# Performance work log

Hardware: AMD Instinct MI355X
Metric: run time of the kernel (lower is better)

Reference implementation:

```python
import jax, jax.numpy as jnp
import numpy as np

NEG_SLOPE = 0.2  # PyG GATv2Conv default
HEADS = 3


def setup_inputs() -> dict:
    key = jax.random.key(0)
    ks = jax.random.split(key, 5)
    N, D, H, C = 16384, 128, HEADS, 128
    x = jax.random.normal(ks[0], (N, D), dtype=jnp.float32)
    Wl = jax.random.normal(ks[1], (D, H * C), dtype=jnp.float32) * (1.0 / np.sqrt(D))
    Wr = jax.random.normal(ks[2], (D, H * C), dtype=jnp.float32) * (1.0 / np.sqrt(D))
    att = jax.random.normal(ks[3], (H, C), dtype=jnp.float32) * (1.0 / np.sqrt(C))
    bias = jnp.zeros((C,), dtype=jnp.float32)
    return {"x": x, "Wl": Wl, "Wr": Wr, "att": att, "bias": bias, "k": 16}


def _knn_indices(x, k):
    # squared euclidean pairwise distances, exclude self (loop=False)
    sq = jnp.sum(x * x, axis=1)
    dist = sq[:, None] + sq[None, :] - 2.0 * (x @ x.T)  # [N, N]
    n = x.shape[0]
    ar = jnp.arange(n)
    dist = dist.at[ar, ar].set(jnp.inf)
    _, idx = jax.lax.top_k(-dist, k)  # [N, k] neighbor (source) indices per target node
    return idx


def reference(x, Wl, Wr, att, bias, k):
    N = x.shape[0]
    H = att.shape[0]
    C = att.shape[1]
    idx = _knn_indices(x, k)                     # [N, k]
    xl = (x @ Wl).reshape(N, H, C)               # source transform
    xr = (x @ Wr).reshape(N, H, C)               # target transform
    xl_nbr = xl[idx]                             # [N, k, H, C] gathered source feats
    g = jax.nn.leaky_relu(xl_nbr + xr[:, None], NEG_SLOPE)
    e = jnp.einsum('nkhc,hc->nkh', g, att)       # per-edge attention logits
    alpha = jax.nn.softmax(e, axis=1)            # softmax over the k neighbors of each target
    out = jnp.einsum('nkh,nkhc->nhc', alpha, xl_nbr)
    return out.mean(axis=1) + bias               # concat=False: mean over heads, then bias
```

## Files before the change

### kernel.cpp

```cpp
#include <hip/hip_runtime.h>
#include <math.h>

#define N_NODES 16384
#define DIM 128
#define HC 384
#define NEG_SLOPE 0.2f
#define KNN 16
#define KP2 6
#define NSEG 8
#define NCAND 192
#define SEGC (N_NODES / NSEG)
#define TILES32 (SEGC / 32)
#define LROW 272
#define LBUF2 (32 * LROW)

typedef _Float16 f16x8 __attribute__((ext_vector_type(8)));
typedef _Float16 f16x2 __attribute__((ext_vector_type(2)));
typedef float f32x4 __attribute__((ext_vector_type(4)));
typedef unsigned long long u64;

__global__ __launch_bounds__(256) void prep_x(const float* __restrict__ x,
                                              float* __restrict__ sq,
                                              _Float16* __restrict__ xhi,
                                              _Float16* __restrict__ xlo) {
  const int wv = threadIdx.x >> 6;
  const int lane = threadIdx.x & 63;
  const int row = blockIdx.x * 4 + wv;
  const float2 v = *(const float2*)&x[row * DIM + lane * 2];
  float s = v.x * v.x + v.y * v.y;
  #pragma unroll
  for (int off = 32; off > 0; off >>= 1) s += __shfl_down(s, off);
  _Float16 h0 = (_Float16)v.x, h1 = (_Float16)v.y;
  _Float16 l0 = (_Float16)(v.x - (float)h0), l1 = (_Float16)(v.y - (float)h1);
  f16x2 hh; hh[0] = h0; hh[1] = h1;
  f16x2 ll; ll[0] = l0; ll[1] = l1;
  *(f16x2*)&xhi[row * DIM + lane * 2] = hh;
  *(f16x2*)&xlo[row * DIM + lane * 2] = ll;
  if (lane == 0) sq[row] = s;
}

__global__ __launch_bounds__(256) void prep_w(const float* __restrict__ Wl,
                                              const float* __restrict__ Wr,
                                              _Float16* __restrict__ wthi,
                                              _Float16* __restrict__ wtlo) {
  const int t = blockIdx.x * 256 + threadIdx.x;
  const int mat = t / 49152;
  const int e = t - mat * 49152;
  const int k = e / HC;
  const int c = e - k * HC;
  const float w = (mat ? Wr : Wl)[e];
  _Float16 h = (_Float16)w;
  _Float16 l = (_Float16)(w - (float)h);
  wthi[mat * 49152 + c * DIM + k] = h;
  wtlo[mat * 49152 + c * DIM + k] = l;
}

__global__ __launch_bounds__(256) void gemm_xw_mfma(const _Float16* __restrict__ xhi,
                                                    const _Float16* __restrict__ xlo,
                                                    const _Float16* __restrict__ wthi,
                                                    const _Float16* __restrict__ wtlo,
                                                    _Float16* __restrict__ xl,
                                                    _Float16* __restrict__ xr) {
  const int lane = threadIdx.x & 63;
  const int wid = blockIdx.x * 4 + (threadIdx.x >> 6);
  const int mat = wid / 6144;
  const int rem = wid - mat * 6144;
  const int rt = rem / 6;
  const int ctg = rem - rt * 6;
  const int r0 = lane & 15;
  const int g8 = (lane >> 4) * 8;

  const _Float16* ap_hi = xhi + (size_t)(rt * 16 + r0) * DIM + g8;
  const _Float16* ap_lo = xlo + (size_t)(rt * 16 + r0) * DIM + g8;
  f16x8 ah[4], al[4];
  #pragma unroll
  for (int ks = 0; ks < 4; ks++) {
    ah[ks] = *(const f16x8*)(ap_hi + ks * 32);
    al[ks] = *(const f16x8*)(ap_lo + ks * 32);
  }
  _Float16* o = mat ? xr : xl;

  #pragma unroll
  for (int ct4 = 0; ct4 < 4; ct4++) {
    const int ct = ctg * 4 + ct4;
    const _Float16* bp_hi = wthi + mat * 49152 + (ct * 16 + r0) * DIM + g8;
    const _Float16* bp_lo = wtlo + mat * 49152 + (ct * 16 + r0) * DIM + g8;
    f32x4 acc = {0.f, 0.f, 0.f, 0.f};
    #pragma unroll
    for (int ks = 0; ks < 4; ks++) {
      f16x8 bh = *(const f16x8*)(bp_hi + ks * 32);
      f16x8 bl = *(const f16x8*)(bp_lo + ks * 32);
      acc = __builtin_amdgcn_mfma_f32_16x16x32_f16(ah[ks], bh, acc, 0, 0, 0);
      acc = __builtin_amdgcn_mfma_f32_16x16x32_f16(ah[ks], bl, acc, 0, 0, 0);
      acc = __builtin_amdgcn_mfma_f32_16x16x32_f16(al[ks], bh, acc, 0, 0, 0);
    }
    #pragma unroll
    for (int i = 0; i < 4; i++) {
      const int row = rt * 16 + (lane >> 4) * 4 + i;
      o[(size_t)row * HC + ct * 16 + r0] = (_Float16)acc[i];
    }
  }
}

__device__ __forceinline__ unsigned umin32(unsigned a, unsigned b) { return a < b ? a : b; }
__device__ __forceinline__ unsigned umax32(unsigned a, unsigned b) { return a > b ? a : b; }

__device__ __forceinline__ void ripple(unsigned pk, unsigned* pool) {
  unsigned cur = pk;
  #pragma unroll
  for (int s = 0; s < KP2; s++) {
    const unsigned mn = umin32(cur, pool[s]);
    cur = umax32(cur, pool[s]);
    pool[s] = mn;
  }
}

__device__ __forceinline__ void insert4s(const f32x4 acc, const f32x4 scv,
                                         int cb_cg, int selfid, unsigned* pool) {
  unsigned k0, k1, k2, k3;
  {
    unsigned kk[4];
    #pragma unroll
    for (int r = 0; r < 4; r++) {
      const int cid = cb_cg + r;
      const float key = fmaf(-2.f, acc[r], scv[r]);
      unsigned u = __float_as_uint(key);
      u ^= (unsigned)(((int)u >> 31) | 0x80000000u);
      unsigned pk = (u & 0xFFFFC000u) | (unsigned)cid;
      kk[r] = (cid == selfid) ? 0xFFFFFFFFu : pk;
    }
    k0 = kk[0]; k1 = kk[1]; k2 = kk[2]; k3 = kk[3];
  }
  #define CSWAP(a, b) { const unsigned mn = umin32(a, b), mx = umax32(a, b); a = mn; b = mx; }
  CSWAP(k0, k1) CSWAP(k2, k3) CSWAP(k0, k2) CSWAP(k1, k3) CSWAP(k1, k2)
  #undef CSWAP
  ripple(k0, pool);
  if (k1 < pool[KP2 - 1]) {
    ripple(k1, pool);
    ripple(k2, pool);
    ripple(k3, pool);
  }
}

__global__ __launch_bounds__(256, 8) void knn_kernel(const _Float16* __restrict__ xhi,
                                                     const float* __restrict__ sq,
                                                     int* __restrict__ cand) {
  __shared__ __align__(16) char lds[2 * LBUF2];

  const int lane = threadIdx.x & 63;
  const int w = threadIdx.x >> 6;
  const int seg = __builtin_amdgcn_readfirstlane(blockIdx.x & 7);
  const int rowgroup = __builtin_amdgcn_readfirstlane((blockIdx.x >> 3) * 4 + w);
  const int rowbase = rowgroup * 16;
  const int segbase = seg * SEGC;
  const int r0 = lane & 15;
  const int g8 = (lane >> 4) * 8;
  const int cg4 = (lane >> 4) * 4;
  const int selfid = rowbase + r0;

  const int st_row = 4 * w + (lane >> 4);
  const int st_chunk = lane & 15;
  const size_t st_src0 = (size_t)st_row * DIM + st_chunk * 8;
  const size_t st_src1 = (size_t)(st_row + 16) * DIM + st_chunk * 8;
  char* const st_dst0 = &lds[st_row * LROW + st_chunk * 16];
  char* const st_dst1 = &lds[(st_row + 16) * LROW + st_chunk * 16];

  f16x8 b[4];
  {
    const size_t rb = (size_t)(rowbase + r0) * DIM + g8;
    #pragma unroll
    for (int ks = 0; ks < 4; ks++) b[ks] = *(const f16x8*)&xhi[rb + ks * 32];
  }

  unsigned pool[KP2];
  #pragma unroll
  for (int j = 0; j < KP2; j++) pool[j] = 0xFFFFFFFFu;

  {
    const float4 g0 = *(const float4*)&xhi[(size_t)segbase * DIM + st_src0];
    const float4 g1 = *(const float4*)&xhi[(size_t)segbase * DIM + st_src1];
    *(float4*)(st_dst0) = g0;
    *(float4*)(st_dst1) = g1;
  }
  f32x4 sA0 = *(const f32x4*)&sq[segbase + cg4];
  f32x4 sA1 = *(const f32x4*)&sq[segbase + 16 + cg4];
  __syncthreads();

  int cur = 0;
  for (int t = 0; t < TILES32; t++) {
    const int tn = (t + 1) & (TILES32 - 1);
    const size_t nb = (size_t)(segbase + tn * 32) * DIM;
    const float4 g0 = *(const float4*)&xhi[nb + st_src0];
    const float4 g1 = *(const float4*)&xhi[nb + st_src1];
    const f32x4 sN0 = *(const f32x4*)&sq[segbase + tn * 32 + cg4];
    const f32x4 sN1 = *(const f32x4*)&sq[segbase + tn * 32 + 16 + cg4];

    const char* rb0 = &lds[cur * LBUF2 + r0 * LROW + g8 * 2];
    const char* rb1 = &lds[cur * LBUF2 + (16 + r0) * LROW + g8 * 2];
    f16x8 a0[4], a1[4];
    #pragma unroll
    for (int ks = 0; ks < 4; ks++) {
      a0[ks] = *(const f16x8*)(rb0 + ks * 64);
      a1[ks] = *(const f16x8*)(rb1 + ks * 64);
    }

    f32x4 acc0 = {0.f, 0.f, 0.f, 0.f};
    f32x4 acc1 = {0.f, 0.f, 0.f, 0.f};
    #pragma unroll
    for (int ks = 0; ks < 4; ks++) {
      acc0 = __builtin_amdgcn_mfma_f32_16x16x32_f16(a0[ks], b[ks], acc0, 0, 0, 0);
      acc1 = __builtin_amdgcn_mfma_f32_16x16x32_f16(a1[ks], b[ks], acc1, 0, 0, 0);
    }

    insert4s(acc0, sA0, segbase + t * 32 + cg4, selfid, pool);
    insert4s(acc1, sA1, segbase + t * 32 + 16 + cg4, selfid, pool);

    *(float4*)(st_dst0 + (cur ^ 1) * LBUF2) = g0;
    *(float4*)(st_dst1 + (cur ^ 1) * LBUF2) = g1;
    __syncthreads();
    sA0 = sN0; sA1 = sN1;
    cur ^= 1;
  }

  const int row = rowbase + r0;
  int* dst = cand + (size_t)row * NCAND + ((lane >> 4) * NSEG + seg) * KP2;
  #pragma unroll
  for (int e = 0; e < KP2; e++) dst[e] = (int)(pool[e] & 0x3FFFu);
}

__device__ __forceinline__ unsigned flip32(float f) {
  unsigned u = __float_as_uint(f);
  return u ^ (unsigned)(((int)u >> 31) | 0x80000000u);
}
__device__ __forceinline__ u64 umin64(u64 a, u64 b) { return a < b ? a : b; }

__global__ __launch_bounds__(256) void refine_kernel(const float* __restrict__ x,
                                                     const float* __restrict__ sq,
                                                     const int* __restrict__ cand,
                                                     int* __restrict__ idxo) {
  __shared__ __align__(16) float Xrow[4][DIM];
  __shared__ u64 Keys[4][NCAND];
  const int wv = threadIdx.x >> 6;
  const int lane = threadIdx.x & 63;
  const int row = blockIdx.x * 4 + wv;

  {
    const float2 v = *(const float2*)&x[(size_t)row * DIM + lane * 2];
    *(float2*)&Xrow[wv][lane * 2] = v;
  }

  const int cs = lane >> 3;
  const int ch8 = lane & 7;
  const int base = row * NCAND;
  const float sr = sq[row];

  #pragma nounroll
  for (int it = 0; it < NCAND / 8; it++) {
    const int ci = it * 8 + cs;
    const int c = cand[base + ci];
    const float4* p = (const float4*)&x[(size_t)c * DIM];
    float d = 0.f;
    #pragma unroll
    for (int j = 0; j < 4; j++) {
      const float4 a = p[ch8 + 8 * j];
      const float4 xv = *(const float4*)&Xrow[wv][(ch8 + 8 * j) * 4];
      d += xv.x * a.x + xv.y * a.y + xv.z * a.z + xv.w * a.w;
    }
    d += __shfl_xor(d, 1);
    d += __shfl_xor(d, 2);
    d += __shfl_xor(d, 4);
    if (ch8 == 0) {
      const float dist = sr + sq[c] - 2.f * d;
      Keys[wv][ci] = ((u64)flip32(dist) << 32) | (unsigned)c;
    }
  }

  u64 k0 = Keys[wv][lane];
  u64 k1 = Keys[wv][64 + lane];
  u64 k2 = Keys[wv][128 + lane];

  int* dst = idxo + (size_t)row * KNN;
  #pragma unroll
  for (int e = 0; e < KNN; e++) {
    u64 m = umin64(k0, umin64(k1, k2));
    #pragma unroll
    for (int off = 32; off > 0; off >>= 1) {
      const u64 o = __shfl_xor(m, off);
      m = umin64(m, o);
    }
    if (k0 == m)      { dst[e] = (int)(unsigned)m; k0 = ~0ull; }
    else if (k1 == m) { dst[e] = (int)(unsigned)m; k1 = ~0ull; }
    else if (k2 == m) { dst[e] = (int)(unsigned)m; k2 = ~0ull; }
  }
}

__global__ __launch_bounds__(256) void attn_kernel(const _Float16* __restrict__ xl,
                                                   const _Float16* __restrict__ xr,
                                                   const float* __restrict__ att,
                                                   const float* __restrict__ bias,
                                                   const int* __restrict__ idxo,
                                                   float* __restrict__ out) {
  const int n = blockIdx.x * 4 + (threadIdx.x >> 6);
  const int lane = threadIdx.x & 63;
  const int ch = lane * 2;
  int myn = 0;
  if (lane < KNN) myn = idxo[(size_t)n * KNN + lane];
  float o0 = 0.f, o1 = 0.f;
  #pragma unroll
  for (int h = 0; h < 3; h++) {
    const f16x2 rr = *(const f16x2*)&xr[(size_t)n * HC + h * 128 + ch];
    const float r0 = (float)rr[0], r1 = (float)rr[1];
    const float2 av = *(const float2*)&att[h * 128 + ch];
    float v0[KNN], v1[KNN], e[KNN];
    #pragma unroll
    for (int kk = 0; kk < KNN; kk++) {
      const f16x2 xv = *(const f16x2*)&xl[(size_t)__shfl(myn, kk) * HC + h * 128 + ch];
      const float x0 = (float)xv[0], x1 = (float)xv[1];
      v0[kk] = x0; v1[kk] = x1;
      float g0 = x0 + r0; g0 = g0 >= 0.f ? g0 : NEG_SLOPE * g0;
      float g1 = x1 + r1; g1 = g1 >= 0.f ? g1 : NEG_SLOPE * g1;
      float p = av.x * g0 + av.y * g1;
      #pragma unroll
      for (int off = 32; off > 0; off >>= 1) p += __shfl_xor(p, off);
      e[kk] = p;
    }
    float m = e[0];
    #pragma unroll
    for (int kk = 1; kk < KNN; kk++) m = fmaxf(m, e[kk]);
    float s = 0.f;
    float w[KNN];
    #pragma unroll
    for (int kk = 0; kk < KNN; kk++) { w[kk] = expf(e[kk] - m); s += w[kk]; }
    #pragma unroll
    for (int kk = 0; kk < KNN; kk++) {
      const float al = w[kk] / s;
      o0 += al * v0[kk];
      o1 += al * v1[kk];
    }
  }
  const float2 bv = *(const float2*)&bias[ch];
  float2 ov;
  ov.x = o0 / 3.f + bv.x;
  ov.y = o1 / 3.f + bv.y;
  *(float2*)&out[(size_t)n * 128 + ch] = ov;
}

extern "C" void kernel_launch(void* const* d_in, const int* in_sizes, int n_in,
                              void* d_out, int out_size, void* d_ws, size_t ws_size,
                              hipStream_t stream) {
  const float* x    = (const float*)d_in[0];
  const float* Wl   = (const float*)d_in[1];
  const float* Wr   = (const float*)d_in[2];
  const float* att  = (const float*)d_in[3];
  const float* bias = (const float*)d_in[4];
  float* out = (float*)d_out;

  _Float16* xhi  = (_Float16*)d_ws;
  _Float16* xlo  = xhi + (size_t)N_NODES * DIM;
  _Float16* wthi = xlo + (size_t)N_NODES * DIM;
  _Float16* wtlo = wthi + 2 * HC * DIM;
  _Float16* xl   = wtlo + 2 * HC * DIM;
  _Float16* xr   = xl + (size_t)N_NODES * HC;
  float*    sqv  = (float*)(xr + (size_t)N_NODES * HC);
  int*      cnd  = (int*)(sqv + N_NODES);
  int*      idx  = cnd + (size_t)N_NODES * NCAND;

  prep_x<<<N_NODES / 4, 256, 0, stream>>>(x, sqv, xhi, xlo);
  prep_w<<<384, 256, 0, stream>>>(Wl, Wr, wthi, wtlo);
  gemm_xw_mfma<<<3072, 256, 0, stream>>>(xhi, xlo, wthi, wtlo, xl, xr);
  knn_kernel<<<(N_NODES / 64) * NSEG, 256, 0, stream>>>(xhi, sqv, cnd);
  refine_kernel<<<N_NODES / 4, 256, 0, stream>>>(x, sqv, cnd, idx);
  attn_kernel<<<N_NODES / 4, 256, 0, stream>>>(xl, xr, att, bias, idx, out);
}
```

Baseline: 407.5 us.

## Process two 16-row query tiles per wave in kNN to reuse LDS candidate tiles

Each wave in the kNN kernel now handles 32 query rows instead of 16, holding two B fragments and two top-k pools. Each candidate tile loaded from LDS feeds four MFMAs instead of two, which halves the grid and the total global and LDS traffic per query row. The cost is higher register pressure, so occupancy is lowered via launch bounds from 8 to 4, and each wave does twice the serial insertion work.

```diff
diff --git a/kernel.cpp b/kernel.cpp
--- a/kernel.cpp
+++ b/kernel.cpp
@@ -142,7 +142,7 @@
   }
 }
 
-__global__ __launch_bounds__(256, 8) void knn_kernel(const _Float16* __restrict__ xhi,
+__global__ __launch_bounds__(256, 4) void knn_kernel(const _Float16* __restrict__ xhi,
                                                      const float* __restrict__ sq,
                                                      int* __restrict__ cand) {
   __shared__ __align__(16) char lds[2 * LBUF2];
@@ -150,13 +150,14 @@
   const int lane = threadIdx.x & 63;
   const int w = threadIdx.x >> 6;
   const int seg = __builtin_amdgcn_readfirstlane(blockIdx.x & 7);
-  const int rowgroup = __builtin_amdgcn_readfirstlane((blockIdx.x >> 3) * 4 + w);
-  const int rowbase = rowgroup * 16;
+  const int blockrow = __builtin_amdgcn_readfirstlane(blockIdx.x >> 3);
+  const int rowbase = blockrow * 128 + w * 32;
   const int segbase = seg * SEGC;
   const int r0 = lane & 15;
   const int g8 = (lane >> 4) * 8;
   const int cg4 = (lane >> 4) * 4;
-  const int selfid = rowbase + r0;
+  const int selfid0 = rowbase + r0;
+  const int selfid1 = rowbase + 16 + r0;
 
   const int st_row = 4 * w + (lane >> 4);
   const int st_chunk = lane & 15;
@@ -165,16 +166,20 @@
   char* const st_dst0 = &lds[st_row * LROW + st_chunk * 16];
   char* const st_dst1 = &lds[(st_row + 16) * LROW + st_chunk * 16];
 
-  f16x8 b[4];
+  f16x8 b_lo[4], b_hi[4];
   {
-    const size_t rb = (size_t)(rowbase + r0) * DIM + g8;
-    #pragma unroll
-    for (int ks = 0; ks < 4; ks++) b[ks] = *(const f16x8*)&xhi[rb + ks * 32];
-  }
-
-  unsigned pool[KP2];
-  #pragma unroll
-  for (int j = 0; j < KP2; j++) pool[j] = 0xFFFFFFFFu;
+    const size_t rb0 = (size_t)(rowbase + r0) * DIM + g8;
+    const size_t rb1 = (size_t)(rowbase + 16 + r0) * DIM + g8;
+    #pragma unroll
+    for (int ks = 0; ks < 4; ks++) {
+      b_lo[ks] = *(const f16x8*)&xhi[rb0 + ks * 32];
+      b_hi[ks] = *(const f16x8*)&xhi[rb1 + ks * 32];
+    }
+  }
+
+  unsigned pool0[KP2], pool1[KP2];
+  #pragma unroll
+  for (int j = 0; j < KP2; j++) { pool0[j] = 0xFFFFFFFFu; pool1[j] = 0xFFFFFFFFu; }
 
   {
     const float4 g0 = *(const float4*)&xhi[(size_t)segbase * DIM + st_src0];
@@ -204,16 +209,23 @@
       a1[ks] = *(const f16x8*)(rb1 + ks * 64);
     }
 
-    f32x4 acc0 = {0.f, 0.f, 0.f, 0.f};
-    f32x4 acc1 = {0.f, 0.f, 0.f, 0.f};
+    f32x4 acc00 = {0.f, 0.f, 0.f, 0.f};
+    f32x4 acc01 = {0.f, 0.f, 0.f, 0.f};
+    f32x4 acc10 = {0.f, 0.f, 0.f, 0.f};
+    f32x4 acc11 = {0.f, 0.f, 0.f, 0.f};
     #pragma unroll
     for (int ks = 0; ks < 4; ks++) {
-      acc0 = __builtin_amdgcn_mfma_f32_16x16x32_f16(a0[ks], b[ks], acc0, 0, 0, 0);
-      acc1 = __builtin_amdgcn_mfma_f32_16x16x32_f16(a1[ks], b[ks], acc1, 0, 0, 0);
-    }
-
-    insert4s(acc0, sA0, segbase + t * 32 + cg4, selfid, pool);
-    insert4s(acc1, sA1, segbase + t * 32 + 16 + cg4, selfid, pool);
+      acc00 = __builtin_amdgcn_mfma_f32_16x16x32_f16(a0[ks], b_lo[ks], acc00, 0, 0, 0);
+      acc01 = __builtin_amdgcn_mfma_f32_16x16x32_f16(a0[ks], b_hi[ks], acc01, 0, 0, 0);
+      acc10 = __builtin_amdgcn_mfma_f32_16x16x32_f16(a1[ks], b_lo[ks], acc10, 0, 0, 0);
+      acc11 = __builtin_amdgcn_mfma_f32_16x16x32_f16(a1[ks], b_hi[ks], acc11, 0, 0, 0);
+    }
+
+    const int cb = segbase + t * 32;
+    insert4s(acc00, sA0, cb + cg4,      selfid0, pool0);
+    insert4s(acc01, sA0, cb + cg4,      selfid1, pool1);
+    insert4s(acc10, sA1, cb + 16 + cg4, selfid0, pool0);
+    insert4s(acc11, sA1, cb + 16 + cg4, selfid1, pool1);
 
     *(float4*)(st_dst0 + (cur ^ 1) * LBUF2) = g0;
     *(float4*)(st_dst1 + (cur ^ 1) * LBUF2) = g1;
@@ -222,10 +234,14 @@
     cur ^= 1;
   }
 
-  const int row = rowbase + r0;
-  int* dst = cand + (size_t)row * NCAND + ((lane >> 4) * NSEG + seg) * KP2;
-  #pragma unroll
-  for (int e = 0; e < KP2; e++) dst[e] = (int)(pool[e] & 0x3FFFu);
+  const int slot = ((lane >> 4) * NSEG + seg) * KP2;
+  int* dst0 = cand + (size_t)(rowbase + r0) * NCAND + slot;
+  int* dst1 = cand + (size_t)(rowbase + 16 + r0) * NCAND + slot;
+  #pragma unroll
+  for (int e = 0; e < KP2; e++) {
+    dst0[e] = (int)(pool0[e] & 0x3FFFu);
+    dst1[e] = (int)(pool1[e] & 0x3FFFu);
+  }
 }
 
 __device__ __forceinline__ unsigned flip32(float f) {
@@ -368,7 +384,7 @@
   prep_x<<<N_NODES / 4, 256, 0, stream>>>(x, sqv, xhi, xlo);
   prep_w<<<384, 256, 0, stream>>>(Wl, Wr, wthi, wtlo);
   gemm_xw_mfma<<<3072, 256, 0, stream>>>(xhi, xlo, wthi, wtlo, xl, xr);
-  knn_kernel<<<(N_NODES / 64) * NSEG, 256, 0, stream>>>(xhi, sqv, cnd);
+  knn_kernel<<<(N_NODES / 128) * NSEG, 256, 0, stream>>>(xhi, sqv, cnd);
   refine_kernel<<<N_NODES / 4, 256, 0, stream>>>(x, sqv, cnd, idx);
   attn_kernel<<<N_NODES / 4, 256, 0, stream>>>(xl, xr, att, bias, idx, out);
 }
```

After: 381.6 us. 6.4% less time.
